# Kernel optimization log

Measured on AMD Instinct MI355X. Metric: run time of the kernel, lower is better.

The kernel has to match this reference:

```python
import jax, jax.numpy as jnp
import numpy as np

D_MODEL = 1024
N_HEAD = 16
D_HEAD = D_MODEL // N_HEAD


def setup_inputs() -> dict:
    key = jax.random.key(0)
    k_x, k_wqkv, k_bqkv, k_wp, k_bp = jax.random.split(key, 5)
    B, T = 2, 2048
    bound = 1.0 / np.sqrt(D_MODEL)
    return {
        "x": jax.random.normal(k_x, (B, T, D_MODEL), dtype=jnp.float32),
        "w_qkv": jax.random.uniform(k_wqkv, (D_MODEL, 3 * D_MODEL), jnp.float32, -bound, bound),
        "b_qkv": jax.random.uniform(k_bqkv, (3 * D_MODEL,), jnp.float32, -bound, bound),
        "w_proj": jax.random.uniform(k_wp, (D_MODEL, D_MODEL), jnp.float32, -bound, bound),
        "b_proj": jax.random.uniform(k_bp, (D_MODEL,), jnp.float32, -bound, bound),
    }


def reference(x, w_qkv, b_qkv, w_proj, b_proj):
    B, T, C = x.shape
    qkv = x @ w_qkv + b_qkv                       # [B,T,3C]
    qkv = qkv.reshape(B, T, 3, N_HEAD, D_HEAD)
    qkv = jnp.transpose(qkv, (2, 0, 3, 1, 4))      # [3,B,H,T,dh]
    q, k, v = qkv[0], qkv[1], qkv[2]
    scale = np.sqrt(D_HEAD).astype(np.float32)
    attn = jnp.einsum("bhqd,bhkd->bhqk", q, k) / scale  # [B,H,T,T]
    causal = jnp.tril(jnp.ones((T, T), dtype=bool))
    attn = jnp.where(causal, attn, -jnp.inf)
    attn = jax.nn.softmax(attn, axis=-1)
    out = jnp.einsum("bhqk,bhkd->bhqd", attn, v)   # [B,H,T,dh]
    out = jnp.transpose(out, (0, 2, 1, 3)).reshape(B, T, C)
    return out @ w_proj + b_proj
```

## Files before the change

kernel.cpp:

```cpp
#include <hip/hip_runtime.h>
#include <hip/hip_bf16.h>
#include <math.h>

constexpr int Bb   = 2;
constexpr int T    = 2048;
constexpr int C    = 1024;
constexpr int H    = 16;
constexpr int M    = Bb * T;
constexpr int NQKV = 3 * C;

typedef __attribute__((ext_vector_type(8))) short bf16x8;
typedef __attribute__((ext_vector_type(4))) float f32x4;

__device__ inline short f2bf(float f) {
    __hip_bfloat16 h = __float2bfloat16(f);
    return *reinterpret_cast<short*>(&h);
}

#if __has_builtin(__builtin_amdgcn_exp2f)
#define EXP2(x) __builtin_amdgcn_exp2f(x)
#else
#define EXP2(x) exp2f(x)
#endif

#define GLOBAL_AS __attribute__((address_space(1)))
#define LDS_AS    __attribute__((address_space(3)))

__device__ __forceinline__ void gload_lds16(const short* g, short* s) {
    __builtin_amdgcn_global_load_lds((const GLOBAL_AS void*)g, (LDS_AS void*)s, 16, 0, 0);
}

__device__ __forceinline__ void lds_fence_wave() {
    __asm__ __volatile__("s_waitcnt lgkmcnt(0)" ::: "memory");
}

__global__ __launch_bounds__(256)
void prep_all(const float* __restrict__ x, short* __restrict__ xb,
              const float* __restrict__ w_qkv, short* __restrict__ wqkvt,
              const float* __restrict__ w_proj, short* __restrict__ wprojt)
{
    __shared__ float tile[32][33];
    const int blk = blockIdx.x;
    const int tid = threadIdx.x;

    if (blk < 4096) {
        const int i = blk * 1024 + tid * 4;
        const float4 v = *(const float4*)(x + i);
        short4 s;
        s.x = f2bf(v.x); s.y = f2bf(v.y); s.z = f2bf(v.z); s.w = f2bf(v.w);
        *(short4*)(xb + i) = s;
        return;
    }

    const bool isqkv = (blk < 7168);
    const int bidx = isqkv ? (blk - 4096) : (blk - 7168);
    const int nblk = isqkv ? 96 : 32;
    const int N    = isqkv ? NQKV : C;
    const float* W = isqkv ? w_qkv : w_proj;
    short* Wt      = isqkv ? wqkvt : wprojt;

    const int n0 = (bidx % nblk) * 32, k0 = (bidx / nblk) * 32;
    const int tx = tid & 31, ty = tid >> 5;
#pragma unroll
    for (int i = 0; i < 32; i += 8)
        tile[ty + i][tx] = W[(size_t)(k0 + ty + i) * N + n0 + tx];
    __syncthreads();
#pragma unroll
    for (int i = 0; i < 32; i += 8)
        Wt[(size_t)(n0 + ty + i) * C + k0 + tx] = f2bf(tile[tx][ty + i]);
}

__global__ __launch_bounds__(256)
void gemm_mfma(const short* __restrict__ A, const short* __restrict__ Bt,
               const float* __restrict__ bias, short* __restrict__ outp,
               int Ndim, int Kdim)
{
    __shared__ __align__(16) short As[128 * 64];
    __shared__ __align__(16) short Bs[128 * 64];

    const int tid = threadIdx.x;
    const int w   = tid >> 6;
    const int l   = tid & 63;
    const int lk  = l & 15;
    const int lq  = l >> 4;
    const int m0  = blockIdx.y * 128, n0 = blockIdx.x * 128;
    const int mw  = (w >> 1) * 64, nw = (w & 1) * 64;

    const int srow = (l >> 3);
    const int scol = (l & 7) * 8;
    const int g0 = w * 16;

    f32x4 acc[4][4];
#pragma unroll
    for (int i = 0; i < 4; ++i)
#pragma unroll
        for (int j = 0; j < 4; ++j) acc[i][j] = (f32x4){0.f, 0.f, 0.f, 0.f};

    for (int k0 = 0; k0 < Kdim; k0 += 64) {
        __syncthreads();
#pragma unroll
        for (int gi = 0; gi < 4; ++gi) {
            const int g = (gi & 1) * 8 + (gi >> 1) * 64 + g0;
            gload_lds16(A  + (size_t)(m0 + g + srow) * Kdim + k0 + scol, &As[g * 64]);
            gload_lds16(Bt + (size_t)(n0 + g + srow) * Kdim + k0 + scol, &Bs[g * 64]);
        }
        __syncthreads();

#pragma unroll
        for (int s = 0; s < 2; ++s) {
            bf16x8 af[4], bfr[4];
#pragma unroll
            for (int mt = 0; mt < 4; ++mt)
                af[mt] = *(const bf16x8*)&As[(mw + mt * 16 + lk) * 64 + s * 32 + lq * 8];
#pragma unroll
            for (int nt = 0; nt < 4; ++nt)
                bfr[nt] = *(const bf16x8*)&Bs[(nw + nt * 16 + lk) * 64 + s * 32 + lq * 8];
#pragma unroll
            for (int mt = 0; mt < 4; ++mt)
#pragma unroll
                for (int nt = 0; nt < 4; ++nt)
                    acc[mt][nt] = __builtin_amdgcn_mfma_f32_16x16x32_bf16(af[mt], bfr[nt], acc[mt][nt], 0, 0, 0);
        }
    }

#pragma unroll
    for (int mt = 0; mt < 4; ++mt) {
#pragma unroll
        for (int nt = 0; nt < 4; ++nt) {
            const int col = n0 + nw + nt * 16 + lk;
            const float bv = bias[col];
#pragma unroll
            for (int r = 0; r < 4; ++r) {
                const int row = m0 + mw + mt * 16 + lq * 4 + r;
                outp[(size_t)row * Ndim + col] = f2bf(acc[mt][nt][r] + bv);
            }
        }
    }
}

__global__ __launch_bounds__(256)
void gemm_mfma_proj(const short* __restrict__ A, const short* __restrict__ Bt,
                    const float* __restrict__ bias, float* __restrict__ outp,
                    int Ndim, int Kdim)
{
    __shared__ __align__(16) short As[64 * 64];
    __shared__ __align__(16) short Bs[128 * 64];

    const int tid = threadIdx.x;
    const int w   = tid >> 6;
    const int l   = tid & 63;
    const int lk  = l & 15;
    const int lq  = l >> 4;
    const int m0  = blockIdx.y * 64, n0 = blockIdx.x * 128;
    const int mw  = (w & 1) * 32, nw = (w >> 1) * 64;

    const int srow = (l >> 3);
    const int scol = (l & 7) * 8;
    const int g0 = w * 16;

    f32x4 acc[2][4];
#pragma unroll
    for (int i = 0; i < 2; ++i)
#pragma unroll
        for (int j = 0; j < 4; ++j) acc[i][j] = (f32x4){0.f, 0.f, 0.f, 0.f};

    for (int k0 = 0; k0 < Kdim; k0 += 64) {
        __syncthreads();
#pragma unroll
        for (int gi = 0; gi < 2; ++gi) {
            const int g = g0 + gi * 8;
            gload_lds16(A + (size_t)(m0 + g + srow) * Kdim + k0 + scol, &As[g * 64]);
        }
#pragma unroll
        for (int gi = 0; gi < 4; ++gi) {
            const int g = (gi & 1) * 8 + (gi >> 1) * 64 + g0;
            gload_lds16(Bt + (size_t)(n0 + g + srow) * Kdim + k0 + scol, &Bs[g * 64]);
        }
        __syncthreads();

#pragma unroll
        for (int s = 0; s < 2; ++s) {
            bf16x8 af[2], bfr[4];
#pragma unroll
            for (int mt = 0; mt < 2; ++mt)
                af[mt] = *(const bf16x8*)&As[(mw + mt * 16 + lk) * 64 + s * 32 + lq * 8];
#pragma unroll
            for (int nt = 0; nt < 4; ++nt)
                bfr[nt] = *(const bf16x8*)&Bs[(nw + nt * 16 + lk) * 64 + s * 32 + lq * 8];
#pragma unroll
            for (int mt = 0; mt < 2; ++mt)
#pragma unroll
                for (int nt = 0; nt < 4; ++nt)
                    acc[mt][nt] = __builtin_amdgcn_mfma_f32_16x16x32_bf16(af[mt], bfr[nt], acc[mt][nt], 0, 0, 0);
        }
    }

#pragma unroll
    for (int mt = 0; mt < 2; ++mt) {
#pragma unroll
        for (int nt = 0; nt < 4; ++nt) {
            const int col = n0 + nw + nt * 16 + lk;
            const float bv = bias[col];
#pragma unroll
            for (int r = 0; r < 4; ++r) {
                const int row = m0 + mw + mt * 16 + lq * 4 + r;
                outp[(size_t)row * Ndim + col] = acc[mt][nt][r] + bv;
            }
        }
    }
}

constexpr int LDV = 136;
constexpr int LDP = 136;
constexpr float SC = 0.18033688f;

__global__ __launch_bounds__(256)
void attn_mfma(const short* __restrict__ qkv, short* __restrict__ att)
{
    __shared__ __align__(16) short Ks[128 * 64];
    __shared__ __align__(16) short Vt[64 * LDV];
    __shared__ __align__(16) short Ps[4][16 * LDP];

    const int idx = blockIdx.x;
    const int xcd = idx & 7;
    const int j   = idx >> 3;
    const int bh  = xcd * 4 + (j & 3);
    const int s   = j >> 2;
    const int qt  = (s < 8)  ? (31 - s)
                  : (s < 16) ? (s - 8)
                  : (s < 24) ? (39 - s)
                  :            (s - 16);
    const int b   = bh >> 4;
    const int h   = bh & 15;
    const int qbase = qt * 64;

    const int tid = threadIdx.x;
    const int w   = tid >> 6;
    const int l   = tid & 63;
    const int lk  = l & 15;
    const int lq  = l >> 4;

    const short* base = qkv + (size_t)b * T * 3072 + h * 64;

    const int q_abs = qbase + w * 16 + lk;
    const short* qp = base + (size_t)q_abs * 3072 + lq * 8;
    const bf16x8 qf0 = *(const bf16x8*)qp;
    const bf16x8 qf1 = *(const bf16x8*)(qp + 32);

    f32x4 acc_o[4];
#pragma unroll
    for (int dt = 0; dt < 4; ++dt) acc_o[dt] = (f32x4){0.f, 0.f, 0.f, 0.f};
    float m_run = -INFINITY;
    float l_run = 0.f;

    const int ksr = l >> 3;
    const int ksc = (l & 7) * 8;

    const int vkg = (tid & 31) * 4;
    const int vd0 = (tid >> 5) * 8;

    const int nkt = (qbase + 64 + 127) >> 7;
#pragma unroll 1
    for (int it = 0; it < nkt; ++it) {
        const int j0 = it * 128;
        __syncthreads();
#pragma unroll
        for (int rr = 0; rr < 4; ++rr) {
            const int g = w * 32 + rr * 8;
            gload_lds16(base + 1024 + (size_t)(j0 + g + ksr) * 3072 + ksc, &Ks[g * 64]);
        }
        {
            const short* vp = base + 2048 + (size_t)(j0 + vkg) * 3072 + vd0;
            bf16x8 vv[4];
#pragma unroll
            for (int kk = 0; kk < 4; ++kk)
                vv[kk] = *(const bf16x8*)(vp + (size_t)kk * 3072);
#pragma unroll
            for (int d = 0; d < 8; ++d) {
                short4 pk;
                pk.x = vv[0][d]; pk.y = vv[1][d]; pk.z = vv[2][d]; pk.w = vv[3][d];
                *(short4*)&Vt[(vd0 + d) * LDV + vkg] = pk;
            }
        }
        __syncthreads();

        f32x4 s4[8];
#pragma unroll
        for (int kt = 0; kt < 8; ++kt) {
            const bf16x8 kf0 = *(const bf16x8*)&Ks[(kt * 16 + lk) * 64 + lq * 8];
            const bf16x8 kf1 = *(const bf16x8*)&Ks[(kt * 16 + lk) * 64 + 32 + lq * 8];
            f32x4 a = (f32x4){0.f, 0.f, 0.f, 0.f};
            a = __builtin_amdgcn_mfma_f32_16x16x32_bf16(kf0, qf0, a, 0, 0, 0);
            a = __builtin_amdgcn_mfma_f32_16x16x32_bf16(kf1, qf1, a, 0, 0, 0);
            s4[kt] = a;
        }

        if (it == nkt - 1) {
#pragma unroll
            for (int kt = 0; kt < 8; ++kt)
#pragma unroll
                for (int r = 0; r < 4; ++r)
                    if (j0 + kt * 16 + lq * 4 + r > q_abs) s4[kt][r] = -1e30f;
        }

        float mx = s4[0][0];
#pragma unroll
        for (int kt = 0; kt < 8; ++kt)
#pragma unroll
            for (int r = 0; r < 4; ++r) mx = fmaxf(mx, s4[kt][r]);
        mx = fmaxf(mx, __shfl_xor(mx, 16));
        mx = fmaxf(mx, __shfl_xor(mx, 32));
        const float mn   = fmaxf(m_run, mx);
        const float corr = EXP2((m_run - mn) * SC);
        m_run = mn;
        const float nmc = -mn * SC;
#pragma unroll
        for (int kt = 0; kt < 8; ++kt)
#pragma unroll
            for (int r = 0; r < 4; ++r)
                s4[kt][r] = EXP2(fmaf(s4[kt][r], SC, nmc));
        float ps = 0.f;
#pragma unroll
        for (int kt = 0; kt < 8; ++kt)
            ps += ((s4[kt][0] + s4[kt][1]) + (s4[kt][2] + s4[kt][3]));
        ps += __shfl_xor(ps, 16);
        ps += __shfl_xor(ps, 32);
        l_run = l_run * corr + ps;

        short* myP = &Ps[w][0];
#pragma unroll
        for (int kt = 0; kt < 8; ++kt) {
            const unsigned int p01 = (unsigned int)(unsigned short)f2bf(s4[kt][0])
                                   | ((unsigned int)(unsigned short)f2bf(s4[kt][1]) << 16);
            const unsigned int p23 = (unsigned int)(unsigned short)f2bf(s4[kt][2])
                                   | ((unsigned int)(unsigned short)f2bf(s4[kt][3]) << 16);
            *(unsigned int*)&myP[lk * LDP + kt * 16 + lq * 4]     = p01;
            *(unsigned int*)&myP[lk * LDP + kt * 16 + lq * 4 + 2] = p23;
        }

        lds_fence_wave();

#pragma unroll
        for (int dt = 0; dt < 4; ++dt)
#pragma unroll
            for (int r = 0; r < 4; ++r) acc_o[dt][r] *= corr;

#pragma unroll
        for (int kc = 0; kc < 4; ++kc) {
            const bf16x8 pf = *(const bf16x8*)&myP[lk * LDP + kc * 32 + lq * 8];
#pragma unroll
            for (int dt = 0; dt < 4; ++dt) {
                const bf16x8 vf = *(const bf16x8*)&Vt[(dt * 16 + lk) * LDV + kc * 32 + lq * 8];
                acc_o[dt] = __builtin_amdgcn_mfma_f32_16x16x32_bf16(vf, pf, acc_o[dt], 0, 0, 0);
            }
        }
    }

    const float inv = 1.f / l_run;
    short* op = att + ((size_t)(b * T + q_abs)) * 1024 + h * 64;
#pragma unroll
    for (int dt = 0; dt < 4; ++dt) {
        short4 pk;
        pk.x = f2bf(acc_o[dt][0] * inv);
        pk.y = f2bf(acc_o[dt][1] * inv);
        pk.z = f2bf(acc_o[dt][2] * inv);
        pk.w = f2bf(acc_o[dt][3] * inv);
        *(short4*)(op + dt * 16 + lq * 4) = pk;
    }
}

extern "C" void kernel_launch(void* const* d_in, const int* in_sizes, int n_in,
                              void* d_out, int out_size, void* d_ws, size_t ws_size,
                              hipStream_t stream)
{
    const float* x      = (const float*)d_in[0];
    const float* w_qkv  = (const float*)d_in[1];
    const float* b_qkv  = (const float*)d_in[2];
    const float* w_proj = (const float*)d_in[3];
    const float* b_proj = (const float*)d_in[4];
    float* out = (float*)d_out;

    short* xb     = (short*)d_ws;
    short* wqkvt  = xb     + (size_t)M * C;
    short* wprojt = wqkvt  + (size_t)NQKV * C;
    short* qkvb   = wprojt + (size_t)C * C;
    short* attb   = qkvb   + (size_t)M * NQKV;

    prep_all<<<8192, 256, 0, stream>>>(x, xb, w_qkv, wqkvt, w_proj, wprojt);
    gemm_mfma<<<dim3(NQKV / 128, M / 128), 256, 0, stream>>>(xb, wqkvt, b_qkv, qkvb, NQKV, C);
    attn_mfma<<<1024, 256, 0, stream>>>(qkvb, attb);
    gemm_mfma_proj<<<dim3(C / 128, M / 64), 256, 0, stream>>>(attb, wprojt, b_proj, out, C, C);
}
```

Before: 205.0 us.

## Halve GEMM K-step to 32 and vectorize epilogue stores via swapped MFMA operands

Both GEMM kernels now stage a K-slice of 32 instead of 64 per iteration, halving shared memory use and simplifying the global-to-LDS load pattern. The MFMA operands are swapped, so each lane holds four consecutive output columns. The epilogue can then write packed short4 / float4 stores with vectorized bias loads instead of scalar strided stores. The trade-off is twice as many barrier-synchronized iterations with less work each. The smaller LDS footprint may allow more resident blocks.

After: 197.8 us. 3.5% less time.

```diff
diff --git a/kernel.cpp b/kernel.cpp
--- a/kernel.cpp
+++ b/kernel.cpp
@@ -75,8 +75,8 @@
                const float* __restrict__ bias, short* __restrict__ outp,
                int Ndim, int Kdim)
 {
-    __shared__ __align__(16) short As[128 * 64];
-    __shared__ __align__(16) short Bs[128 * 64];
+    __shared__ __align__(16) short As[128 * 32];
+    __shared__ __align__(16) short Bs[128 * 32];
 
     const int tid = threadIdx.x;
     const int w   = tid >> 6;
@@ -86,9 +86,12 @@
     const int m0  = blockIdx.y * 128, n0 = blockIdx.x * 128;
     const int mw  = (w >> 1) * 64, nw = (w & 1) * 64;
 
-    const int srow = (l >> 3);
-    const int scol = (l & 7) * 8;
-    const int g0 = w * 16;
+    const int srow = w * 16 + (l >> 2);
+    const int scol = (l & 3) * 8;
+    short* asdst0 = &As[w * 512];
+    short* asdst1 = &As[2048 + w * 512];
+    short* bsdst0 = &Bs[w * 512];
+    short* bsdst1 = &Bs[2048 + w * 512];
 
     f32x4 acc[4][4];
 #pragma unroll
@@ -96,44 +99,43 @@
 #pragma unroll
         for (int j = 0; j < 4; ++j) acc[i][j] = (f32x4){0.f, 0.f, 0.f, 0.f};
 
-    for (int k0 = 0; k0 < Kdim; k0 += 64) {
-        __syncthreads();
-#pragma unroll
-        for (int gi = 0; gi < 4; ++gi) {
-            const int g = (gi & 1) * 8 + (gi >> 1) * 64 + g0;
-            gload_lds16(A  + (size_t)(m0 + g + srow) * Kdim + k0 + scol, &As[g * 64]);
-            gload_lds16(Bt + (size_t)(n0 + g + srow) * Kdim + k0 + scol, &Bs[g * 64]);
-        }
-        __syncthreads();
-
-#pragma unroll
-        for (int s = 0; s < 2; ++s) {
-            bf16x8 af[4], bfr[4];
-#pragma unroll
-            for (int mt = 0; mt < 4; ++mt)
-                af[mt] = *(const bf16x8*)&As[(mw + mt * 16 + lk) * 64 + s * 32 + lq * 8];
+    for (int k0 = 0; k0 < Kdim; k0 += 32) {
+        __syncthreads();
+        gload_lds16(A  + (size_t)(m0 + srow)      * Kdim + k0 + scol, asdst0);
+        gload_lds16(A  + (size_t)(m0 + 64 + srow) * Kdim + k0 + scol, asdst1);
+        gload_lds16(Bt + (size_t)(n0 + srow)      * Kdim + k0 + scol, bsdst0);
+        gload_lds16(Bt + (size_t)(n0 + 64 + srow) * Kdim + k0 + scol, bsdst1);
+        __syncthreads();
+
+        bf16x8 af[4], bfr[4];
+#pragma unroll
+        for (int mt = 0; mt < 4; ++mt)
+            af[mt] = *(const bf16x8*)&As[(mw + mt * 16 + lk) * 32 + lq * 8];
+#pragma unroll
+        for (int nt = 0; nt < 4; ++nt)
+            bfr[nt] = *(const bf16x8*)&Bs[(nw + nt * 16 + lk) * 32 + lq * 8];
+#pragma unroll
+        for (int mt = 0; mt < 4; ++mt)
 #pragma unroll
             for (int nt = 0; nt < 4; ++nt)
-                bfr[nt] = *(const bf16x8*)&Bs[(nw + nt * 16 + lk) * 64 + s * 32 + lq * 8];
-#pragma unroll
-            for (int mt = 0; mt < 4; ++mt)
-#pragma unroll
-                for (int nt = 0; nt < 4; ++nt)
-                    acc[mt][nt] = __builtin_amdgcn_mfma_f32_16x16x32_bf16(af[mt], bfr[nt], acc[mt][nt], 0, 0, 0);
-        }
-    }
-
+                acc[mt][nt] = __builtin_amdgcn_mfma_f32_16x16x32_bf16(bfr[nt], af[mt], acc[mt][nt], 0, 0, 0);
+    }
+
+    float4 bv[4];
+#pragma unroll
+    for (int nt = 0; nt < 4; ++nt)
+        bv[nt] = *(const float4*)(bias + n0 + nw + nt * 16 + lq * 4);
 #pragma unroll
     for (int mt = 0; mt < 4; ++mt) {
+        short* rowp = outp + (size_t)(m0 + mw + mt * 16 + lk) * Ndim + n0 + nw + lq * 4;
 #pragma unroll
         for (int nt = 0; nt < 4; ++nt) {
-            const int col = n0 + nw + nt * 16 + lk;
-            const float bv = bias[col];
-#pragma unroll
-            for (int r = 0; r < 4; ++r) {
-                const int row = m0 + mw + mt * 16 + lq * 4 + r;
-                outp[(size_t)row * Ndim + col] = f2bf(acc[mt][nt][r] + bv);
-            }
+            short4 pk;
+            pk.x = f2bf(acc[mt][nt][0] + bv[nt].x);
+            pk.y = f2bf(acc[mt][nt][1] + bv[nt].y);
+            pk.z = f2bf(acc[mt][nt][2] + bv[nt].z);
+            pk.w = f2bf(acc[mt][nt][3] + bv[nt].w);
+            *(short4*)(rowp + nt * 16) = pk;
         }
     }
 }
@@ -143,8 +145,8 @@
                     const float* __restrict__ bias, float* __restrict__ outp,
                     int Ndim, int Kdim)
 {
-    __shared__ __align__(16) short As[64 * 64];
-    __shared__ __align__(16) short Bs[128 * 64];
+    __shared__ __align__(16) short As[64 * 32];
+    __shared__ __align__(16) short Bs[128 * 32];
 
     const int tid = threadIdx.x;
     const int w   = tid >> 6;
@@ -154,9 +156,11 @@
     const int m0  = blockIdx.y * 64, n0 = blockIdx.x * 128;
     const int mw  = (w & 1) * 32, nw = (w >> 1) * 64;
 
-    const int srow = (l >> 3);
-    const int scol = (l & 7) * 8;
-    const int g0 = w * 16;
+    const int srow = w * 16 + (l >> 2);
+    const int scol = (l & 3) * 8;
+    short* asdst  = &As[w * 512];
+    short* bsdst0 = &Bs[w * 512];
+    short* bsdst1 = &Bs[2048 + w * 512];
 
     f32x4 acc[2][4];
 #pragma unroll
@@ -164,48 +168,42 @@
 #pragma unroll
         for (int j = 0; j < 4; ++j) acc[i][j] = (f32x4){0.f, 0.f, 0.f, 0.f};
 
-    for (int k0 = 0; k0 < Kdim; k0 += 64) {
-        __syncthreads();
-#pragma unroll
-        for (int gi = 0; gi < 2; ++gi) {
-            const int g = g0 + gi * 8;
-            gload_lds16(A + (size_t)(m0 + g + srow) * Kdim + k0 + scol, &As[g * 64]);
-        }
-#pragma unroll
-        for (int gi = 0; gi < 4; ++gi) {
-            const int g = (gi & 1) * 8 + (gi >> 1) * 64 + g0;
-            gload_lds16(Bt + (size_t)(n0 + g + srow) * Kdim + k0 + scol, &Bs[g * 64]);
-        }
-        __syncthreads();
-
-#pragma unroll
-        for (int s = 0; s < 2; ++s) {
-            bf16x8 af[2], bfr[4];
-#pragma unroll
-            for (int mt = 0; mt < 2; ++mt)
-                af[mt] = *(const bf16x8*)&As[(mw + mt * 16 + lk) * 64 + s * 32 + lq * 8];
+    for (int k0 = 0; k0 < Kdim; k0 += 32) {
+        __syncthreads();
+        gload_lds16(A  + (size_t)(m0 + srow)      * Kdim + k0 + scol, asdst);
+        gload_lds16(Bt + (size_t)(n0 + srow)      * Kdim + k0 + scol, bsdst0);
+        gload_lds16(Bt + (size_t)(n0 + 64 + srow) * Kdim + k0 + scol, bsdst1);
+        __syncthreads();
+
+        bf16x8 af[2], bfr[4];
+#pragma unroll
+        for (int mt = 0; mt < 2; ++mt)
+            af[mt] = *(const bf16x8*)&As[(mw + mt * 16 + lk) * 32 + lq * 8];
+#pragma unroll
+        for (int nt = 0; nt < 4; ++nt)
+            bfr[nt] = *(const bf16x8*)&Bs[(nw + nt * 16 + lk) * 32 + lq * 8];
+#pragma unroll
+        for (int mt = 0; mt < 2; ++mt)
 #pragma unroll
             for (int nt = 0; nt < 4; ++nt)
-                bfr[nt] = *(const bf16x8*)&Bs[(nw + nt * 16 + lk) * 64 + s * 32 + lq * 8];
-#pragma unroll
-            for (int mt = 0; mt < 2; ++mt)
-#pragma unroll
-                for (int nt = 0; nt < 4; ++nt)
-                    acc[mt][nt] = __builtin_amdgcn_mfma_f32_16x16x32_bf16(af[mt], bfr[nt], acc[mt][nt], 0, 0, 0);
-        }
-    }
-
+                acc[mt][nt] = __builtin_amdgcn_mfma_f32_16x16x32_bf16(bfr[nt], af[mt], acc[mt][nt], 0, 0, 0);
+    }
+
+    float4 bv[4];
+#pragma unroll
+    for (int nt = 0; nt < 4; ++nt)
+        bv[nt] = *(const float4*)(bias + n0 + nw + nt * 16 + lq * 4);
 #pragma unroll
     for (int mt = 0; mt < 2; ++mt) {
+        float* rowp = outp + (size_t)(m0 + mw + mt * 16 + lk) * Ndim + n0 + nw + lq * 4;
 #pragma unroll
         for (int nt = 0; nt < 4; ++nt) {
-            const int col = n0 + nw + nt * 16 + lk;
-            const float bv = bias[col];
-#pragma unroll
-            for (int r = 0; r < 4; ++r) {
-                const int row = m0 + mw + mt * 16 + lq * 4 + r;
-                outp[(size_t)row * Ndim + col] = acc[mt][nt][r] + bv;
-            }
+            float4 v;
+            v.x = acc[mt][nt][0] + bv[nt].x;
+            v.y = acc[mt][nt][1] + bv[nt].y;
+            v.z = acc[mt][nt][2] + bv[nt].z;
+            v.w = acc[mt][nt][3] + bv[nt].w;
+            *(float4*)(rowp + nt * 16) = v;
         }
     }
 }
```
